# Kernel optimization log

Measured on AMD Instinct MI355X. Metric: run time of the kernel, lower is better.

Reference implementation:

```python
import jax, jax.numpy as jnp
import numpy as np

LAYER_NUMS = 3
# activations per layer: elu, elu, none (matches expert_activations=["elu","elu",null])
ACTS = [jax.nn.elu, jax.nn.elu, None]


def setup_inputs() -> dict:
    key = jax.random.key(0)
    k1, k2, k3, k4 = jax.random.split(key, 4)
    E, D, B_ = 8, 2048, 4096
    weight_blend = jax.random.uniform(k1, (E,), dtype=jnp.float32)
    x = jax.random.normal(k2, (B_, D), dtype=jnp.float32)
    W = jax.random.normal(k3, (LAYER_NUMS, E, D, D), dtype=jnp.float32) * 0.02
    B = jax.random.normal(k4, (LAYER_NUMS, D), dtype=jnp.float32) * 0.02
    return {"weight_blend": weight_blend, "x": x, "W": W, "B": B}


def reference(weight_blend, x, W, B):
    # Dropout is identity in eval/deterministic mode (expert_keep_prob=0.0).
    for i in range(LAYER_NUMS):
        # blended weight: sum_e c_e * W_e  -> (out, in)
        w = jnp.einsum("e,eoi->oi", weight_blend, W[i])
        x = x @ w.T + B[i]
        if ACTS[i] is not None:
            x = ACTS[i](x)
    return x
```

## Files before the change

### kernel.cpp

```cpp
#include <hip/hip_runtime.h>
#include <hip/hip_bf16.h>

#define MDIM 4096
#define NDIM 2048
#define KDIM 2048
#define KTILES 32

typedef __attribute__((ext_vector_type(8))) short bf16x8;
typedef __attribute__((ext_vector_type(4))) float f32x4;

__device__ __forceinline__ unsigned short f2bf(float f) {
    unsigned u = __builtin_bit_cast(unsigned, f);
    u += 0x7FFFu + ((u >> 16) & 1u);
    return (unsigned short)(u >> 16);
}

__global__ __launch_bounds__(256) void blend_convert_kernel(
    const float* __restrict__ W, const float* __restrict__ cb,
    const float* __restrict__ x,
    unsigned short* __restrict__ wb, unsigned short* __restrict__ xb)
{
    float c[8];
#pragma unroll
    for (int e = 0; e < 8; ++e) c[e] = cb[e];
    const unsigned per_layer = 4194304u;
    const unsigned wtotal4 = 3u * (per_layer >> 2);
    const unsigned xtotal4 = 2097152u;
    const unsigned total = wtotal4 + xtotal4;
    unsigned stride = gridDim.x * blockDim.x;
    for (unsigned i = blockIdx.x * blockDim.x + threadIdx.x; i < total; i += stride) {
        if (i < wtotal4) {
            unsigned layer = i >> 20;
            unsigned off = (i & 1048575u) << 2;
            const float* base = W + (size_t)layer * 8u * per_layer + off;
            float4 s = make_float4(0.f, 0.f, 0.f, 0.f);
#pragma unroll
            for (int e = 0; e < 8; ++e) {
                float4 v = *(const float4*)(base + (size_t)e * per_layer);
                s.x += c[e] * v.x; s.y += c[e] * v.y;
                s.z += c[e] * v.z; s.w += c[e] * v.w;
            }
            ushort4 o;
            o.x = f2bf(s.x); o.y = f2bf(s.y); o.z = f2bf(s.z); o.w = f2bf(s.w);
            *(ushort4*)(wb + (size_t)layer * per_layer + off) = o;
        } else {
            unsigned j = (i - wtotal4) << 2;
            float4 v = *(const float4*)(x + j);
            ushort4 o;
            o.x = f2bf(v.x); o.y = f2bf(v.y); o.z = f2bf(v.z); o.w = f2bf(v.w);
            *(ushort4*)(xb + j) = o;
        }
    }
}

#define BARR() do { asm volatile("" ::: "memory"); __builtin_amdgcn_s_barrier(); asm volatile("" ::: "memory"); } while (0)
#define SP(N) __builtin_amdgcn_s_setprio(N)
#define VMC(N) asm volatile("s_waitcnt vmcnt(" #N ")" ::: "memory")

template<int ACT, typename OutT>
__global__ __launch_bounds__(512, 2) void gemm_bn128(
    const unsigned short* __restrict__ A,
    const unsigned short* __restrict__ Bw,
    const float* __restrict__ bias,
    OutT* __restrict__ C)
{
    __shared__ __align__(16) unsigned short lds[73728];
    char* ldsc = (char*)lds;

    const int tid = threadIdx.x;
    const int wid = tid >> 6;
    const int lane = tid & 63;
    const int wr = wid >> 2;
    const int wc = wid & 3;

    const int wg = (blockIdx.x & 7) * 32 + (blockIdx.x >> 3);
    const size_t blockM = (size_t)(wg & 15) * 256;
    const size_t blockN = (size_t)(wg >> 4) * 128;

    const int sw = (lane & 7) << 4;
    const int ck = (lane >> 4) << 4;
    const int rAb = wr * 64 + (lane & 15);
    const int rBb = wc * 32 + (lane & 15);

    const int srow = tid >> 3;
    const int scol = ((tid & 7) ^ (srow & 7)) << 3;
    const unsigned short* aStage = A + (blockM + srow) * KDIM + scol;
    const unsigned short* bStage = Bw + (blockN + srow) * KDIM + scol;

#define STAGE_AS(BUF, S, KT) do { \
    const unsigned short* g_ = aStage + (size_t)(S) * 64 * KDIM + (size_t)(KT) * 64; \
    __builtin_amdgcn_global_load_lds((const __attribute__((address_space(1))) void*)g_, \
        (__attribute__((address_space(3))) void*)(ldsc + (BUF) * 49152 + (S) * 8192 + tid * 16), \
        16, 0, 0); \
} while (0)

#define STAGE_BS(BUF, S, KT) do { \
    const unsigned short* g_ = bStage + (size_t)(S) * 64 * KDIM + (size_t)(KT) * 64; \
    __builtin_amdgcn_global_load_lds((const __attribute__((address_space(1))) void*)g_, \
        (__attribute__((address_space(3))) void*)(ldsc + (BUF) * 49152 + 32768 + (S) * 8192 + tid * 16), \
        16, 0, 0); \
} while (0)

#define RD_A(BUF, QM, M, KK) \
    (*(const bf16x8*)(ldsc + (BUF) * 49152 + ((QM) * 128 + rAb + (M) * 16) * 128 + (((KK) * 64 + ck) ^ sw)))
#define RD_B(BUF, N, KK) \
    (*(const bf16x8*)(ldsc + (BUF) * 49152 + 32768 + (rBb + (N) * 16) * 128 + (((KK) * 64 + ck) ^ sw)))

    f32x4 acc[2][4][2];
#pragma unroll
    for (int q = 0; q < 2; ++q)
#pragma unroll
        for (int m = 0; m < 4; ++m)
#pragma unroll
            for (int n = 0; n < 2; ++n) acc[q][m][n] = (f32x4){0.f, 0.f, 0.f, 0.f};

    bf16x8 af[4][2], bfr[2][2];

#define READ_AQ(BUF, QM) do { _Pragma("unroll") for (int m_ = 0; m_ < 4; ++m_) { \
    af[m_][0] = RD_A(BUF, QM, m_, 0); af[m_][1] = RD_A(BUF, QM, m_, 1); } } while (0)
#define READ_BF(BUF) do { \
    bfr[0][0] = RD_B(BUF, 0, 0); bfr[0][1] = RD_B(BUF, 0, 1); \
    bfr[1][0] = RD_B(BUF, 1, 0); bfr[1][1] = RD_B(BUF, 1, 1); } while (0)
#define DO_MFMA16(QM) do { _Pragma("unroll") for (int m_ = 0; m_ < 4; ++m_) \
    _Pragma("unroll") for (int n_ = 0; n_ < 2; ++n_) { \
        acc[QM][m_][n_] = __builtin_amdgcn_mfma_f32_16x16x32_bf16(af[m_][0], bfr[n_][0], acc[QM][m_][n_], 0, 0, 0); \
        acc[QM][m_][n_] = __builtin_amdgcn_mfma_f32_16x16x32_bf16(af[m_][1], bfr[n_][1], acc[QM][m_][n_], 0, 0, 0); } } while (0)

    STAGE_AS(0, 0, 0); STAGE_AS(0, 1, 0); STAGE_AS(0, 2, 0); STAGE_AS(0, 3, 0);
    STAGE_BS(0, 0, 0); STAGE_BS(0, 1, 0);
    STAGE_AS(1, 0, 1); STAGE_AS(1, 1, 1); STAGE_AS(1, 2, 1); STAGE_AS(1, 3, 1);
    STAGE_BS(1, 0, 1); STAGE_BS(1, 1, 1);
    VMC(6);
    BARR();

    int cur = 0;
#pragma unroll 1
    for (int t = 0; t < KTILES; ++t) {
        int stb = cur + 2; if (stb >= 3) stb -= 3;
        const int t1 = t + 1, t2 = t + 2;
        READ_AQ(cur, 0);
        READ_BF(cur);
        if (t2 < KTILES) { STAGE_AS(stb, 0, t2); STAGE_AS(stb, 1, t2); STAGE_BS(stb, 0, t2); }
        BARR(); SP(1); DO_MFMA16(0); SP(0); BARR();
        READ_AQ(cur, 1);
        if (t2 < KTILES) { STAGE_AS(stb, 2, t2); STAGE_AS(stb, 3, t2); STAGE_BS(stb, 1, t2); }
        BARR(); SP(1); DO_MFMA16(1); SP(0);
        if (t2 < KTILES) { VMC(6); }
        else if (t1 < KTILES) { VMC(0); }
        BARR();
        cur = cur + 1; if (cur >= 3) cur = 0;
    }

    const int crow = (lane >> 4) * 4;
    const int ccol = lane & 15;
#pragma unroll
    for (int qm = 0; qm < 2; ++qm)
#pragma unroll
        for (int m = 0; m < 4; ++m)
#pragma unroll
            for (int n = 0; n < 2; ++n) {
                const size_t col = blockN + wc * 32 + n * 16 + ccol;
                const float bv = bias[col];
#pragma unroll
                for (int r = 0; r < 4; ++r) {
                    const size_t row = blockM + qm * 128 + wr * 64 + m * 16 + crow + r;
                    float v = acc[qm][m][n][r] + bv;
                    if (ACT) v = v > 0.f ? v : expm1f(v);
                    if constexpr (sizeof(OutT) == 2) {
                        C[row * NDIM + col] = (OutT)f2bf(v);
                    } else {
                        C[row * NDIM + col] = (OutT)v;
                    }
                }
            }
#undef STAGE_AS
#undef STAGE_BS
#undef RD_A
#undef RD_B
#undef READ_AQ
#undef READ_BF
#undef DO_MFMA16
}

extern "C" void kernel_launch(void* const* d_in, const int* in_sizes, int n_in,
                              void* d_out, int out_size, void* d_ws, size_t ws_size,
                              hipStream_t stream) {
    const float* blendw = (const float*)d_in[0];
    const float* x      = (const float*)d_in[1];
    const float* W      = (const float*)d_in[2];
    const float* Bb     = (const float*)d_in[3];
    float* out = (float*)d_out;

    unsigned short* wb = (unsigned short*)d_ws;
    unsigned short* xb = wb + (size_t)3 * 4194304;
    unsigned short* y0 = xb + 8388608;
    unsigned short* y1 = xb;

    blend_convert_kernel<<<2048, 256, 0, stream>>>(W, blendw, x, wb, xb);

    const int grid = (MDIM / 256) * (NDIM / 128);
    gemm_bn128<1, unsigned short><<<grid, 512, 0, stream>>>(xb, wb,               Bb,        y0);
    gemm_bn128<1, unsigned short><<<grid, 512, 0, stream>>>(y0, wb + 4194304,     Bb + 2048, y1);
    gemm_bn128<0, float        ><<<grid, 512, 0, stream>>>(y1, wb + 2 * 4194304,  Bb + 4096, out);
}
```

Before: 238.5 us.

## Switch GEMM wave layout to 4x2 with 64x64 per-wave tiles

Each of the 8 waves now covers a 64x64 output tile (4x2 wave grid) instead of two 64x32 sub-tiles split across two half-iterations. Per k-tile, a wave reads A and B fragments once, issues all staging loads, and runs 32 MFMAs in a single phase, which removes the intermediate barriers. This is meant to raise register-level reuse and cut LDS reads per MFMA. The cost is more live fragment registers per wave and less interleaving between loads and compute.

```diff
diff --git a/kernel.cpp b/kernel.cpp
--- a/kernel.cpp
+++ b/kernel.cpp
@@ -70,8 +70,8 @@
     const int tid = threadIdx.x;
     const int wid = tid >> 6;
     const int lane = tid & 63;
-    const int wr = wid >> 2;
-    const int wc = wid & 3;
+    const int wr = wid >> 1;
+    const int wc = wid & 1;
 
     const int wg = (blockIdx.x & 7) * 32 + (blockIdx.x >> 3);
     const size_t blockM = (size_t)(wg & 15) * 256;
@@ -80,7 +80,7 @@
     const int sw = (lane & 7) << 4;
     const int ck = (lane >> 4) << 4;
     const int rAb = wr * 64 + (lane & 15);
-    const int rBb = wc * 32 + (lane & 15);
+    const int rBb = wc * 64 + (lane & 15);
 
     const int srow = tid >> 3;
     const int scol = ((tid & 7) ^ (srow & 7)) << 3;
@@ -101,30 +101,16 @@
         16, 0, 0); \
 } while (0)
 
-#define RD_A(BUF, QM, M, KK) \
-    (*(const bf16x8*)(ldsc + (BUF) * 49152 + ((QM) * 128 + rAb + (M) * 16) * 128 + (((KK) * 64 + ck) ^ sw)))
+#define RD_A(BUF, M, KK) \
+    (*(const bf16x8*)(ldsc + (BUF) * 49152 + ((rAb + (M) * 16)) * 128 + (((KK) * 64 + ck) ^ sw)))
 #define RD_B(BUF, N, KK) \
     (*(const bf16x8*)(ldsc + (BUF) * 49152 + 32768 + (rBb + (N) * 16) * 128 + (((KK) * 64 + ck) ^ sw)))
 
-    f32x4 acc[2][4][2];
+    f32x4 acc[4][4];
 #pragma unroll
-    for (int q = 0; q < 2; ++q)
+    for (int m = 0; m < 4; ++m)
 #pragma unroll
-        for (int m = 0; m < 4; ++m)
-#pragma unroll
-            for (int n = 0; n < 2; ++n) acc[q][m][n] = (f32x4){0.f, 0.f, 0.f, 0.f};
-
-    bf16x8 af[4][2], bfr[2][2];
-
-#define READ_AQ(BUF, QM) do { _Pragma("unroll") for (int m_ = 0; m_ < 4; ++m_) { \
-    af[m_][0] = RD_A(BUF, QM, m_, 0); af[m_][1] = RD_A(BUF, QM, m_, 1); } } while (0)
-#define READ_BF(BUF) do { \
-    bfr[0][0] = RD_B(BUF, 0, 0); bfr[0][1] = RD_B(BUF, 0, 1); \
-    bfr[1][0] = RD_B(BUF, 1, 0); bfr[1][1] = RD_B(BUF, 1, 1); } while (0)
-#define DO_MFMA16(QM) do { _Pragma("unroll") for (int m_ = 0; m_ < 4; ++m_) \
-    _Pragma("unroll") for (int n_ = 0; n_ < 2; ++n_) { \
-        acc[QM][m_][n_] = __builtin_amdgcn_mfma_f32_16x16x32_bf16(af[m_][0], bfr[n_][0], acc[QM][m_][n_], 0, 0, 0); \
-        acc[QM][m_][n_] = __builtin_amdgcn_mfma_f32_16x16x32_bf16(af[m_][1], bfr[n_][1], acc[QM][m_][n_], 0, 0, 0); } } while (0)
+        for (int n = 0; n < 4; ++n) acc[m][n] = (f32x4){0.f, 0.f, 0.f, 0.f};
 
     STAGE_AS(0, 0, 0); STAGE_AS(0, 1, 0); STAGE_AS(0, 2, 0); STAGE_AS(0, 3, 0);
     STAGE_BS(0, 0, 0); STAGE_BS(0, 1, 0);
@@ -138,13 +124,25 @@
     for (int t = 0; t < KTILES; ++t) {
         int stb = cur + 2; if (stb >= 3) stb -= 3;
         const int t1 = t + 1, t2 = t + 2;
-        READ_AQ(cur, 0);
-        READ_BF(cur);
-        if (t2 < KTILES) { STAGE_AS(stb, 0, t2); STAGE_AS(stb, 1, t2); STAGE_BS(stb, 0, t2); }
-        BARR(); SP(1); DO_MFMA16(0); SP(0); BARR();
-        READ_AQ(cur, 1);
-        if (t2 < KTILES) { STAGE_AS(stb, 2, t2); STAGE_AS(stb, 3, t2); STAGE_BS(stb, 1, t2); }
-        BARR(); SP(1); DO_MFMA16(1); SP(0);
+        bf16x8 af[4][2], bf[4][2];
+#pragma unroll
+        for (int m = 0; m < 4; ++m) { af[m][0] = RD_A(cur, m, 0); af[m][1] = RD_A(cur, m, 1); }
+#pragma unroll
+        for (int n = 0; n < 4; ++n) { bf[n][0] = RD_B(cur, n, 0); bf[n][1] = RD_B(cur, n, 1); }
+        if (t2 < KTILES) {
+            STAGE_AS(stb, 0, t2); STAGE_AS(stb, 1, t2); STAGE_AS(stb, 2, t2); STAGE_AS(stb, 3, t2);
+            STAGE_BS(stb, 0, t2); STAGE_BS(stb, 1, t2);
+        }
+        SP(1);
+#pragma unroll
+        for (int kk = 0; kk < 2; ++kk)
+#pragma unroll
+            for (int m = 0; m < 4; ++m)
+#pragma unroll
+                for (int n = 0; n < 4; ++n)
+                    acc[m][n] = __builtin_amdgcn_mfma_f32_16x16x32_bf16(
+                        af[m][kk], bf[n][kk], acc[m][n], 0, 0, 0);
+        SP(0);
         if (t2 < KTILES) { VMC(6); }
         else if (t1 < KTILES) { VMC(0); }
         BARR();
@@ -154,32 +152,27 @@
     const int crow = (lane >> 4) * 4;
     const int ccol = lane & 15;
 #pragma unroll
-    for (int qm = 0; qm < 2; ++qm)
+    for (int m = 0; m < 4; ++m)
 #pragma unroll
-        for (int m = 0; m < 4; ++m)
+        for (int n = 0; n < 4; ++n) {
+            const size_t col = blockN + wc * 64 + n * 16 + ccol;
+            const float bv = bias[col];
 #pragma unroll
-            for (int n = 0; n < 2; ++n) {
-                const size_t col = blockN + wc * 32 + n * 16 + ccol;
-                const float bv = bias[col];
-#pragma unroll
-                for (int r = 0; r < 4; ++r) {
-                    const size_t row = blockM + qm * 128 + wr * 64 + m * 16 + crow + r;
-                    float v = acc[qm][m][n][r] + bv;
-                    if (ACT) v = v > 0.f ? v : expm1f(v);
-                    if constexpr (sizeof(OutT) == 2) {
-                        C[row * NDIM + col] = (OutT)f2bf(v);
-                    } else {
-                        C[row * NDIM + col] = (OutT)v;
-                    }
+            for (int r = 0; r < 4; ++r) {
+                const size_t row = blockM + wr * 64 + m * 16 + crow + r;
+                float v = acc[m][n][r] + bv;
+                if (ACT) v = v > 0.f ? v : expm1f(v);
+                if constexpr (sizeof(OutT) == 2) {
+                    C[row * NDIM + col] = (OutT)f2bf(v);
+                } else {
+                    C[row * NDIM + col] = (OutT)v;
                 }
             }
+        }
 #undef STAGE_AS
 #undef STAGE_BS
 #undef RD_A
 #undef RD_B
-#undef READ_AQ
-#undef READ_BF
-#undef DO_MFMA16
 }
 
 extern "C" void kernel_launch(void* const* d_in, const int* in_sizes, int n_in,
```

Result: faster. 232.2 us (-2.7%).
